# Kernel optimization log

Measured on AMD Instinct MI355X. Metric: run time of the kernel, lower is better.

The kernel has to match this reference:

```python
import jax, jax.numpy as jnp
import numpy as np

EMBED, HEADS, LEVELS, POINTS = 256, 8, 1, 4


def setup_inputs():
    key = jax.random.key(0)
    ks = jax.random.split(key, 8)
    B, NQ = 8, 8192
    Hh, Ww = 128, 128
    E, Hn, L, P = EMBED, HEADS, LEVELS, POINTS
    s = 1.0 / np.sqrt(E)
    return dict(
        query=jax.random.normal(ks[0], (B, NQ, E), jnp.float32),
        value=jax.random.normal(ks[1], (B, Hh * Ww, E), jnp.float32),
        ref_2d=jax.random.uniform(ks[2], (B, NQ, L, 2), dtype=jnp.float32),
        spatial_shapes=jnp.array([[Hh, Ww]], dtype=jnp.int32),
        W_off=jax.random.normal(ks[3], (E, Hn * L * P * 2), jnp.float32) * 0.01,
        b_off=jax.random.normal(ks[4], (Hn * L * P * 2,), jnp.float32) * 0.5,
        W_attn=jax.random.normal(ks[5], (E, Hn * L * P), jnp.float32) * s,
        b_attn=jnp.zeros((Hn * L * P,), jnp.float32),
        W_val=jax.random.normal(ks[6], (E, E), jnp.float32) * s,
        b_val=jnp.zeros((E,), jnp.float32),
        W_out=jax.random.normal(ks[7], (E, E), jnp.float32) * s,
        b_out=jnp.zeros((E,), jnp.float32),
    )


def _bilinear_sample(v, loc, Hl, Wl):
    # v: (B, Hn, Hl*Wl, dh); loc: (B, Hn, NQ, P, 2) normalized [0,1] (x, y)
    B, Hn, NQ, P, _ = loc.shape
    dh = v.shape[-1]
    # torch grid_sample(align_corners=False) pixel coords: p = loc * size - 0.5
    x = loc[..., 0] * Wl - 0.5
    y = loc[..., 1] * Hl - 0.5
    x0 = jnp.floor(x); y0 = jnp.floor(y)
    x1 = x0 + 1.0; y1 = y0 + 1.0
    wx1 = x - x0; wx0 = 1.0 - wx1
    wy1 = y - y0; wy0 = 1.0 - wy1

    def corner(xc, yc, w):
        valid = (xc >= 0) & (xc < Wl) & (yc >= 0) & (yc < Hl)  # zeros padding
        xi = jnp.clip(xc, 0, Wl - 1).astype(jnp.int32)
        yi = jnp.clip(yc, 0, Hl - 1).astype(jnp.int32)
        idx = (yi * Wl + xi).reshape(B, Hn, NQ * P, 1)
        vals = jnp.take_along_axis(v, idx, axis=2).reshape(B, Hn, NQ, P, dh)
        return vals * (w * valid.astype(v.dtype))[..., None]

    return (corner(x0, y0, wx0 * wy0) + corner(x1, y0, wx1 * wy0)
            + corner(x0, y1, wx0 * wy1) + corner(x1, y1, wx1 * wy1))


def _forward(query, value, ref_2d, W_off, b_off, W_attn, b_attn, W_val, b_val, W_out, b_out, shapes):
    B, NQ, E = query.shape
    Hn, L, P = HEADS, LEVELS, POINTS
    dh = E // Hn
    NV = value.shape[1]
    identity = query
    v = (value @ W_val + b_val).reshape(B, NV, Hn, dh)
    off = (query @ W_off + b_off).reshape(B, NQ, Hn, L, P, 2)
    attn = jax.nn.softmax((query @ W_attn + b_attn).reshape(B, NQ, Hn, L * P), axis=-1)
    attn = attn.reshape(B, NQ, Hn, L, P)
    # offset_normalizer = (W, H) per level
    norm = jnp.asarray(shapes[:, ::-1].copy(), dtype=query.dtype)
    loc = ref_2d[:, :, None, :, None, :] + off / norm[None, None, None, :, None, :]
    loc = jnp.transpose(loc, (0, 2, 1, 3, 4, 5))   # (B, Hn, NQ, L, P, 2)
    attn_t = jnp.transpose(attn, (0, 2, 1, 3, 4))  # (B, Hn, NQ, L, P)
    v_t = jnp.transpose(v, (0, 2, 1, 3))           # (B, Hn, NV, dh)
    starts = np.concatenate([[0], np.cumsum(shapes[:, 0] * shapes[:, 1])]).astype(np.int64)
    out = jnp.zeros((B, Hn, NQ, dh), query.dtype)
    for l in range(L):  # static small loop over feature levels
        Hl, Wl = int(shapes[l, 0]), int(shapes[l, 1])
        v_l = v_t[:, :, int(starts[l]):int(starts[l + 1]), :]
        samp = _bilinear_sample(v_l, loc[:, :, :, l], Hl, Wl)  # (B,Hn,NQ,P,dh)
        out = out + jnp.sum(samp * attn_t[:, :, :, l, :, None], axis=3)
    out = jnp.transpose(out, (0, 2, 1, 3)).reshape(B, NQ, E)
    # dropout is identity at eval time
    return out @ W_out + b_out + identity


def reference(query, value, ref_2d, spatial_shapes, W_off, b_off, W_attn, b_attn, W_val, b_val, W_out, b_out):
    shapes = np.asarray(jax.device_get(spatial_shapes))  # static level shapes
    return _forward(query, value, ref_2d, W_off, b_off, W_attn, b_attn, W_val, b_val, W_out, b_out, shapes)
```

## Files before the change

### kernel.cpp

```cpp
#include <hip/hip_runtime.h>

typedef short s16x8 __attribute__((ext_vector_type(8)));
typedef float f32x4 __attribute__((ext_vector_type(4)));

#define HN 8
#define PP 4
#define DH 32
#define NQc 8192
#define NVc 16384
#define EE 256
#define HWc 128

__device__ __forceinline__ unsigned short f2bf(float x) {
  unsigned u = __float_as_uint(x);
  u += 0x7FFF + ((u >> 16) & 1);
  return (unsigned short)(u >> 16);
}
__device__ __forceinline__ float bf2f(unsigned short h) {
  return __uint_as_float(((unsigned)h) << 16);
}

__global__ __launch_bounds__(256) void wprep(
    const float* __restrict__ Wval, const float* __restrict__ Wout,
    const float* __restrict__ Woff, const float* __restrict__ Wattn,
    const float* __restrict__ boff, const float* __restrict__ battn,
    unsigned short* __restrict__ wvt, unsigned short* __restrict__ wot,
    unsigned short* __restrict__ wct, float* __restrict__ bcat) {
  int g = blockIdx.x * 256 + threadIdx.x;
  if (g < 65536) {
    int n = g >> 8, k = g & 255;
    wvt[n * 256 + k] = f2bf(Wval[k * 256 + n]);
  } else if (g < 131072) {
    int g2 = g - 65536;
    int n = g2 >> 8, k = g2 & 255;
    wot[n * 256 + k] = f2bf(Wout[k * 256 + n]);
  } else if (g < 163840) {
    int g2 = g - 131072;
    int n = g2 >> 8, k = g2 & 255;
    float v = 0.f;
    if (n < 64) v = Woff[k * 64 + n];
    else if (n < 96) v = Wattn[k * 32 + (n - 64)];
    wct[n * 256 + k] = f2bf(v);
  } else if (g < 163968) {
    int c = g - 163840;
    bcat[c] = (c < 64) ? boff[c] : ((c < 96) ? battn[c - 64] : 0.f);
  }
}

#define MODE_VAL 0
#define MODE_PLAIN 1
#define MODE_OUT 2

template <int MODE>
struct SmemBytes { static constexpr int v = 36864; };
template <> struct SmemBytes<MODE_PLAIN> { static constexpr int v = 49664; };
template <> struct SmemBytes<MODE_OUT>   { static constexpr int v = 33792; };

template <int MODE, bool ABF16>
__global__ __launch_bounds__(256) void mfma_gemm(
    const void* __restrict__ Ain, const unsigned short* __restrict__ Wt,
    const float* __restrict__ bias, const float* __restrict__ resid,
    const float* __restrict__ ref2d, unsigned int* __restrict__ meta,
    void* __restrict__ outp) {
  __shared__ __align__(16) char smem[SmemBytes<MODE>::v];
  unsigned short* As = (unsigned short*)smem;
  unsigned short* Ws = As + 128 * 40;
  const int t = threadIdx.x;
  const int lane = t & 63, wave = t >> 6;
  const int lane15 = lane & 15, quad = lane >> 4;
  const int wr = wave >> 1, wc = wave & 1;
  const int bm = blockIdx.x * 128, bn = blockIdx.y * 128;

  f32x4 acc[4][4];
#pragma unroll
  for (int i = 0; i < 4; ++i)
#pragma unroll
    for (int j = 0; j < 4; ++j)
#pragma unroll
      for (int r = 0; r < 4; ++r) acc[i][j][r] = 0.f;

  const int ar = t >> 3, ac = (t & 7) * 4;
  const int wr2 = t >> 1, wcp = (t & 1) * 2;

  for (int k0 = 0; k0 < 256; k0 += 32) {
    float4 av[4];
    uint4 ab0, ab1;
    if (!ABF16) {
      const float* Af = (const float*)Ain;
#pragma unroll
      for (int i = 0; i < 4; ++i)
        av[i] = *(const float4*)(Af + (size_t)(bm + ar + i * 32) * 256 + k0 + ac);
    } else {
      const unsigned short* Ab = (const unsigned short*)Ain;
      ab0 = *(const uint4*)(Ab + (size_t)(bm + wr2) * 256 + k0 + wcp * 8);
      ab1 = *(const uint4*)(Ab + (size_t)(bm + wr2) * 256 + k0 + wcp * 8 + 8);
    }
    uint4 wv0 = *(const uint4*)(Wt + (size_t)(bn + wr2) * 256 + k0 + wcp * 8);
    uint4 wv1 = *(const uint4*)(Wt + (size_t)(bn + wr2) * 256 + k0 + wcp * 8 + 8);
    __syncthreads();
    if (!ABF16) {
#pragma unroll
      for (int i = 0; i < 4; ++i) {
        ushort4 c;
        c.x = f2bf(av[i].x); c.y = f2bf(av[i].y); c.z = f2bf(av[i].z); c.w = f2bf(av[i].w);
        *(ushort4*)&As[(ar + i * 32) * 40 + ac] = c;
      }
    } else {
      *(uint4*)&As[wr2 * 40 + wcp * 8] = ab0;
      *(uint4*)&As[wr2 * 40 + wcp * 8 + 8] = ab1;
    }
    *(uint4*)&Ws[wr2 * 40 + wcp * 8] = wv0;
    *(uint4*)&Ws[wr2 * 40 + wcp * 8 + 8] = wv1;
    __syncthreads();
    s16x8 af[4], bfr[4];
#pragma unroll
    for (int tm = 0; tm < 4; ++tm)
      af[tm] = *(const s16x8*)&As[(wr * 64 + tm * 16 + lane15) * 40 + quad * 8];
#pragma unroll
    for (int tn = 0; tn < 4; ++tn)
      bfr[tn] = *(const s16x8*)&Ws[(wc * 64 + tn * 16 + lane15) * 40 + quad * 8];
#pragma unroll
    for (int tm = 0; tm < 4; ++tm)
#pragma unroll
      for (int tn = 0; tn < 4; ++tn)
        acc[tm][tn] = __builtin_amdgcn_mfma_f32_16x16x32_bf16(af[tm], bfr[tn], acc[tm][tn], 0, 0, 0);
  }

  if (MODE == MODE_VAL) {
    unsigned short* Ct = (unsigned short*)smem;
    __syncthreads();
#pragma unroll
    for (int tm = 0; tm < 4; ++tm)
#pragma unroll
      for (int tn = 0; tn < 4; ++tn) {
        const int coll = wc * 64 + tn * 16 + lane15;
        const float bcol = bias[bn + coll];
#pragma unroll
        for (int r = 0; r < 4; ++r) {
          const int rowl = wr * 64 + tm * 16 + quad * 4 + r;
          Ct[rowl * 144 + coll] = f2bf(acc[tm][tn][r] + bcol);
        }
      }
    __syncthreads();
    unsigned short* outs = (unsigned short*)outp;
    const int b = bm >> 14, n0 = bm & (NVc - 1), hbase = bn >> 5;
#pragma unroll
    for (int i = 0; i < 8; ++i) {
      const int id = i * 256 + t;
      const int h4 = id >> 9, rem = id & 511, n = rem >> 2, c4 = rem & 3;
      uint4 v = *(const uint4*)&Ct[n * 144 + h4 * 32 + c4 * 8];
      *(uint4*)(outs + (((size_t)(b * HN + hbase + h4) * NVc + n0 + n) * DH + c4 * 8)) = v;
    }
  } else if (MODE == MODE_PLAIN) {
    float* Cf = (float*)smem;
    __syncthreads();
#pragma unroll
    for (int tm = 0; tm < 4; ++tm)
#pragma unroll
      for (int tn = 0; tn < 4; ++tn) {
        const int coll = wc * 64 + tn * 16 + lane15;
        if (coll < 96) {
          const float bcol = bias[coll];
#pragma unroll
          for (int r = 0; r < 4; ++r) {
            const int rowl = wr * 64 + tm * 16 + quad * 4 + r;
            Cf[rowl * 97 + coll] = acc[tm][tn][r] + bcol;
          }
        }
      }
    __syncthreads();
#pragma unroll
    for (int i = 0; i < 4; ++i) {
      const int task = i * 256 + t;
      const int h = task & 7, rowl = task >> 3;
      const int bq = bm + rowl;
      const float* row = Cf + rowl * 97;
      const float rx = ref2d[(size_t)bq * 2 + 0];
      const float ry = ref2d[(size_t)bq * 2 + 1];
      const float l0 = row[64 + h * 4 + 0], l1 = row[64 + h * 4 + 1];
      const float l2 = row[64 + h * 4 + 2], l3 = row[64 + h * 4 + 3];
      const float mx = fmaxf(fmaxf(l0, l1), fmaxf(l2, l3));
      float e0 = __expf(l0 - mx), e1 = __expf(l1 - mx), e2 = __expf(l2 - mx), e3 = __expf(l3 - mx);
      const float inv = 1.0f / (e0 + e1 + e2 + e3);
      float ee[4] = {e0, e1, e2, e3};
      unsigned int* m = meta + ((size_t)bq * 8 + h) * 20;
      uint4 pk;
      float4 wts[4];
#pragma unroll
      for (int p = 0; p < PP; ++p) {
        const float a = ee[p] * inv;
        const float ox = row[h * 8 + p * 2 + 0];
        const float oy = row[h * 8 + p * 2 + 1];
        const float x = (rx + ox * (1.0f / HWc)) * (float)HWc - 0.5f;
        const float y = (ry + oy * (1.0f / HWc)) * (float)HWc - 0.5f;
        const float x0f = floorf(x), y0f = floorf(y);
        const int x0 = (int)x0f, y0 = (int)y0f;
        const float wx1 = x - x0f, wx0 = 1.f - wx1;
        const float wy1 = y - y0f, wy0 = 1.f - wy1;
        const bool vx0 = (unsigned)x0 < (unsigned)HWc, vx1 = (unsigned)(x0 + 1) < (unsigned)HWc;
        const bool vy0 = (unsigned)y0 < (unsigned)HWc, vy1 = (unsigned)(y0 + 1) < (unsigned)HWc;
        const int xi0 = min(max(x0, 0), HWc - 1), xi1 = min(max(x0 + 1, 0), HWc - 1);
        const int yi0 = min(max(y0, 0), HWc - 1), yi1 = min(max(y0 + 1, 0), HWc - 1);
        const unsigned pv = (unsigned)xi0 | ((unsigned)yi0 << 8) | ((unsigned)xi1 << 16) | ((unsigned)yi1 << 24);
        if (p == 0) pk.x = pv; else if (p == 1) pk.y = pv; else if (p == 2) pk.z = pv; else pk.w = pv;
        float4 w;
        w.x = (vx0 && vy0) ? a * wx0 * wy0 : 0.f;
        w.y = (vx1 && vy0) ? a * wx1 * wy0 : 0.f;
        w.z = (vx0 && vy1) ? a * wx0 * wy1 : 0.f;
        w.w = (vx1 && vy1) ? a * wx1 * wy1 : 0.f;
        wts[p] = w;
      }
      *(uint4*)m = pk;
#pragma unroll
      for (int p = 0; p < PP; ++p) *(float4*)&m[4 + p * 4] = wts[p];
    }
  } else {
    float* Cf = (float*)smem;
    float* outf = (float*)outp;
#pragma unroll
    for (int pass = 0; pass < 2; ++pass) {
      __syncthreads();
      if (wr == pass) {
#pragma unroll
        for (int tm = 0; tm < 4; ++tm)
#pragma unroll
          for (int tn = 0; tn < 4; ++tn) {
            const int coll = wc * 64 + tn * 16 + lane15;
            const float bcol = bias[bn + coll];
#pragma unroll
            for (int r = 0; r < 4; ++r) {
              const int rowl = tm * 16 + quad * 4 + r;
              Cf[rowl * 132 + coll] = acc[tm][tn][r] + bcol;
            }
          }
      }
      __syncthreads();
#pragma unroll
      for (int i = 0; i < 8; ++i) {
        const int id = i * 256 + t;
        const int n = id >> 5, c = id & 31;
        const size_t row = (size_t)bm + pass * 64 + n;
        float4 v = *(const float4*)&Cf[n * 132 + c * 4];
        float4 rs = *(const float4*)(resid + row * 256 + bn + c * 4);
        v.x += rs.x; v.y += rs.y; v.z += rs.z; v.w += rs.w;
        *(float4*)(outf + row * 256 + bn + c * 4) = v;
      }
    }
  }
}

__global__ __launch_bounds__(256) void sample_kernel(
    const unsigned short* __restrict__ vbuf,
    const unsigned int* __restrict__ meta,
    unsigned short* __restrict__ outs) {
  const int t = threadIdx.x;
  const int d4 = (t & 7) << 2;
  const int ql = t >> 3;
  const int sl = blockIdx.x >> 8;
  const int qc = blockIdx.x & 255;
  const int b = sl >> 3;
  const int h = sl & 7;
  const int q = qc * 32 + ql;
  const size_t bq = (size_t)b * NQc + q;
  const unsigned int* m = meta + ((size_t)bq * 8 + h) * 20;
  const uint4 pk = *(const uint4*)m;
  const unsigned short* vb = vbuf + (size_t)sl * (NVc * DH) + d4;

  float4 acc = {0.f, 0.f, 0.f, 0.f};
#pragma unroll
  for (int p = 0; p < PP; ++p) {
    const unsigned P = (p == 0) ? pk.x : (p == 1) ? pk.y : (p == 2) ? pk.z : pk.w;
    const float4 w = *(const float4*)(m + 4 + p * 4);
    const int x0 = P & 255, y0 = (P >> 8) & 255, x1 = (P >> 16) & 255, y1 = P >> 24;
    const int r0 = y0 << 12, r1 = y1 << 12;
    const ushort4 v00 = *(const ushort4*)(vb + r0 + (x0 << 5));
    const ushort4 v10 = *(const ushort4*)(vb + r0 + (x1 << 5));
    const ushort4 v01 = *(const ushort4*)(vb + r1 + (x0 << 5));
    const ushort4 v11 = *(const ushort4*)(vb + r1 + (x1 << 5));
    acc.x += w.x * bf2f(v00.x); acc.y += w.x * bf2f(v00.y);
    acc.z += w.x * bf2f(v00.z); acc.w += w.x * bf2f(v00.w);
    acc.x += w.y * bf2f(v10.x); acc.y += w.y * bf2f(v10.y);
    acc.z += w.y * bf2f(v10.z); acc.w += w.y * bf2f(v10.w);
    acc.x += w.z * bf2f(v01.x); acc.y += w.z * bf2f(v01.y);
    acc.z += w.z * bf2f(v01.z); acc.w += w.z * bf2f(v01.w);
    acc.x += w.w * bf2f(v11.x); acc.y += w.w * bf2f(v11.y);
    acc.z += w.w * bf2f(v11.z); acc.w += w.w * bf2f(v11.w);
  }
  ushort4 o;
  o.x = f2bf(acc.x); o.y = f2bf(acc.y); o.z = f2bf(acc.z); o.w = f2bf(acc.w);
  *(ushort4*)(outs + bq * EE + h * DH + d4) = o;
}

extern "C" void kernel_launch(void* const* d_in, const int* in_sizes, int n_in,
                              void* d_out, int out_size, void* d_ws, size_t ws_size,
                              hipStream_t stream) {
  const float* query = (const float*)d_in[0];
  const float* value = (const float*)d_in[1];
  const float* ref2d = (const float*)d_in[2];
  const float* Woff  = (const float*)d_in[4];
  const float* boff  = (const float*)d_in[5];
  const float* Wattn = (const float*)d_in[6];
  const float* battn = (const float*)d_in[7];
  const float* Wval  = (const float*)d_in[8];
  const float* bval  = (const float*)d_in[9];
  const float* Wout  = (const float*)d_in[10];
  const float* bout  = (const float*)d_in[11];
  float* out = (float*)d_out;

  unsigned short* vbuf = (unsigned short*)d_ws;
  unsigned int* meta   = (unsigned int*)(vbuf + 33554432);
  unsigned short* sbuf = (unsigned short*)(meta + 10485760);
  unsigned short* wvt  = sbuf + 16777216;
  unsigned short* wot  = wvt + 65536;
  unsigned short* wct  = wot + 65536;
  float* bcat          = (float*)(wct + 32768);

  wprep<<<641, 256, 0, stream>>>(Wval, Wout, Woff, Wattn, boff, battn, wvt, wot, wct, bcat);

  mfma_gemm<MODE_VAL, false><<<dim3(1024, 2), 256, 0, stream>>>(
      (const void*)value, wvt, bval, nullptr, nullptr, nullptr, (void*)vbuf);

  mfma_gemm<MODE_PLAIN, false><<<dim3(512, 1), 256, 0, stream>>>(
      (const void*)query, wct, bcat, nullptr, ref2d, meta, nullptr);

  sample_kernel<<<16384, 256, 0, stream>>>(vbuf, meta, sbuf);

  mfma_gemm<MODE_OUT, true><<<dim3(512, 2), 256, 0, stream>>>(
      (const void*)sbuf, wot, bout, query, nullptr, nullptr, (void*)out);
}
```

Before: 417.2 us.

## Prefetch next K tile and write GEMM epilogues directly from transposed accumulators

The GEMM main loop now issues the global loads for the next K-slice right after the LDS barrier, so memory latency overlaps the MFMA work on the current slice. The MFMA operands are swapped so each lane holds four consecutive output columns of one row. This lets the value and output epilogues store vectorized results straight to global memory without staging through LDS and extra barriers. Shared memory shrinks for those modes, and the plain mode uses a padded float4-aligned stride. Holding the prefetched tile costs extra registers, and the direct stores may coalesce less well than the staged writes.

```diff
diff --git a/kernel.cpp b/kernel.cpp
--- a/kernel.cpp
+++ b/kernel.cpp
@@ -52,9 +52,8 @@
 #define MODE_OUT 2
 
 template <int MODE>
-struct SmemBytes { static constexpr int v = 36864; };
-template <> struct SmemBytes<MODE_PLAIN> { static constexpr int v = 49664; };
-template <> struct SmemBytes<MODE_OUT>   { static constexpr int v = 33792; };
+struct SmemBytes { static constexpr int v = 20480; };
+template <> struct SmemBytes<MODE_PLAIN> { static constexpr int v = 51200; };
 
 template <int MODE, bool ABF16>
 __global__ __launch_bounds__(256) void mfma_gemm(
@@ -82,21 +81,28 @@
   const int ar = t >> 3, ac = (t & 7) * 4;
   const int wr2 = t >> 1, wcp = (t & 1) * 2;
 
+  float4 av[4];
+  uint4 ab0, ab1, wv0, wv1;
+
+#define LOAD_TILE(K0)                                                          \
+  do {                                                                         \
+    if (!ABF16) {                                                              \
+      const float* Af = (const float*)Ain;                                     \
+      _Pragma("unroll") for (int i = 0; i < 4; ++i)                            \
+          av[i] = *(const float4*)(Af + (size_t)(bm + ar + i * 32) * 256 +     \
+                                   (K0) + ac);                                 \
+    } else {                                                                   \
+      const unsigned short* Ab = (const unsigned short*)Ain;                   \
+      ab0 = *(const uint4*)(Ab + (size_t)(bm + wr2) * 256 + (K0) + wcp * 8);   \
+      ab1 = *(const uint4*)(Ab + (size_t)(bm + wr2) * 256 + (K0) + wcp * 8 + 8); \
+    }                                                                          \
+    wv0 = *(const uint4*)(Wt + (size_t)(bn + wr2) * 256 + (K0) + wcp * 8);     \
+    wv1 = *(const uint4*)(Wt + (size_t)(bn + wr2) * 256 + (K0) + wcp * 8 + 8); \
+  } while (0)
+
+  LOAD_TILE(0);
+
   for (int k0 = 0; k0 < 256; k0 += 32) {
-    float4 av[4];
-    uint4 ab0, ab1;
-    if (!ABF16) {
-      const float* Af = (const float*)Ain;
-#pragma unroll
-      for (int i = 0; i < 4; ++i)
-        av[i] = *(const float4*)(Af + (size_t)(bm + ar + i * 32) * 256 + k0 + ac);
-    } else {
-      const unsigned short* Ab = (const unsigned short*)Ain;
-      ab0 = *(const uint4*)(Ab + (size_t)(bm + wr2) * 256 + k0 + wcp * 8);
-      ab1 = *(const uint4*)(Ab + (size_t)(bm + wr2) * 256 + k0 + wcp * 8 + 8);
-    }
-    uint4 wv0 = *(const uint4*)(Wt + (size_t)(bn + wr2) * 256 + k0 + wcp * 8);
-    uint4 wv1 = *(const uint4*)(Wt + (size_t)(bn + wr2) * 256 + k0 + wcp * 8 + 8);
     __syncthreads();
     if (!ABF16) {
 #pragma unroll
@@ -112,6 +118,7 @@
     *(uint4*)&Ws[wr2 * 40 + wcp * 8] = wv0;
     *(uint4*)&Ws[wr2 * 40 + wcp * 8 + 8] = wv1;
     __syncthreads();
+    if (k0 < 224) LOAD_TILE(k0 + 32);
     s16x8 af[4], bfr[4];
 #pragma unroll
     for (int tm = 0; tm < 4; ++tm)
@@ -123,58 +130,57 @@
     for (int tm = 0; tm < 4; ++tm)
 #pragma unroll
       for (int tn = 0; tn < 4; ++tn)
-        acc[tm][tn] = __builtin_amdgcn_mfma_f32_16x16x32_bf16(af[tm], bfr[tn], acc[tm][tn], 0, 0, 0);
+        acc[tm][tn] = __builtin_amdgcn_mfma_f32_16x16x32_bf16(bfr[tn], af[tm], acc[tm][tn], 0, 0, 0);
   }
+#undef LOAD_TILE
 
   if (MODE == MODE_VAL) {
-    unsigned short* Ct = (unsigned short*)smem;
-    __syncthreads();
-#pragma unroll
-    for (int tm = 0; tm < 4; ++tm)
-#pragma unroll
-      for (int tn = 0; tn < 4; ++tn) {
-        const int coll = wc * 64 + tn * 16 + lane15;
-        const float bcol = bias[bn + coll];
-#pragma unroll
-        for (int r = 0; r < 4; ++r) {
-          const int rowl = wr * 64 + tm * 16 + quad * 4 + r;
-          Ct[rowl * 144 + coll] = f2bf(acc[tm][tn][r] + bcol);
-        }
-      }
-    __syncthreads();
     unsigned short* outs = (unsigned short*)outp;
-    const int b = bm >> 14, n0 = bm & (NVc - 1), hbase = bn >> 5;
-#pragma unroll
-    for (int i = 0; i < 8; ++i) {
-      const int id = i * 256 + t;
-      const int h4 = id >> 9, rem = id & 511, n = rem >> 2, c4 = rem & 3;
-      uint4 v = *(const uint4*)&Ct[n * 144 + h4 * 32 + c4 * 8];
-      *(uint4*)(outs + (((size_t)(b * HN + hbase + h4) * NVc + n0 + n) * DH + c4 * 8)) = v;
+    const size_t b = (size_t)(bm >> 14);
+    const int n0 = bm & (NVc - 1);
+#pragma unroll
+    for (int tn = 0; tn < 4; ++tn) {
+      const int ch0 = bn + wc * 64 + tn * 16 + quad * 4;
+      const float4 b4 = *(const float4*)&bias[ch0];
+      const int h = ch0 >> 5, dh0 = ch0 & 31;
+#pragma unroll
+      for (int tm = 0; tm < 4; ++tm) {
+        const int n = n0 + wr * 64 + tm * 16 + lane15;
+        ushort4 o;
+        o.x = f2bf(acc[tm][tn][0] + b4.x);
+        o.y = f2bf(acc[tm][tn][1] + b4.y);
+        o.z = f2bf(acc[tm][tn][2] + b4.z);
+        o.w = f2bf(acc[tm][tn][3] + b4.w);
+        *(ushort4*)(outs + ((b * HN + h) * NVc + n) * DH + dh0) = o;
+      }
     }
   } else if (MODE == MODE_PLAIN) {
     float* Cf = (float*)smem;
     __syncthreads();
 #pragma unroll
-    for (int tm = 0; tm < 4; ++tm)
-#pragma unroll
-      for (int tn = 0; tn < 4; ++tn) {
-        const int coll = wc * 64 + tn * 16 + lane15;
-        if (coll < 96) {
-          const float bcol = bias[coll];
-#pragma unroll
-          for (int r = 0; r < 4; ++r) {
-            const int rowl = wr * 64 + tm * 16 + quad * 4 + r;
-            Cf[rowl * 97 + coll] = acc[tm][tn][r] + bcol;
-          }
+    for (int tn = 0; tn < 4; ++tn) {
+      const int col0 = wc * 64 + tn * 16 + quad * 4;
+      if (col0 < 96) {
+        const float4 b4 = *(const float4*)&bias[col0];
+#pragma unroll
+        for (int tm = 0; tm < 4; ++tm) {
+          const int m = wr * 64 + tm * 16 + lane15;
+          float4 v;
+          v.x = acc[tm][tn][0] + b4.x;
+          v.y = acc[tm][tn][1] + b4.y;
+          v.z = acc[tm][tn][2] + b4.z;
+          v.w = acc[tm][tn][3] + b4.w;
+          *(float4*)&Cf[m * 100 + col0] = v;
         }
       }
+    }
     __syncthreads();
 #pragma unroll
     for (int i = 0; i < 4; ++i) {
       const int task = i * 256 + t;
       const int h = task & 7, rowl = task >> 3;
       const int bq = bm + rowl;
-      const float* row = Cf + rowl * 97;
+      const float* row = Cf + rowl * 100;
       const float rx = ref2d[(size_t)bq * 2 + 0];
       const float ry = ref2d[(size_t)bq * 2 + 1];
       const float l0 = row[64 + h * 4 + 0], l1 = row[64 + h * 4 + 1];
@@ -215,35 +221,21 @@
       for (int p = 0; p < PP; ++p) *(float4*)&m[4 + p * 4] = wts[p];
     }
   } else {
-    float* Cf = (float*)smem;
     float* outf = (float*)outp;
 #pragma unroll
-    for (int pass = 0; pass < 2; ++pass) {
-      __syncthreads();
-      if (wr == pass) {
-#pragma unroll
-        for (int tm = 0; tm < 4; ++tm)
-#pragma unroll
-          for (int tn = 0; tn < 4; ++tn) {
-            const int coll = wc * 64 + tn * 16 + lane15;
-            const float bcol = bias[bn + coll];
-#pragma unroll
-            for (int r = 0; r < 4; ++r) {
-              const int rowl = tm * 16 + quad * 4 + r;
-              Cf[rowl * 132 + coll] = acc[tm][tn][r] + bcol;
-            }
-          }
-      }
-      __syncthreads();
-#pragma unroll
-      for (int i = 0; i < 8; ++i) {
-        const int id = i * 256 + t;
-        const int n = id >> 5, c = id & 31;
-        const size_t row = (size_t)bm + pass * 64 + n;
-        float4 v = *(const float4*)&Cf[n * 132 + c * 4];
-        float4 rs = *(const float4*)(resid + row * 256 + bn + c * 4);
-        v.x += rs.x; v.y += rs.y; v.z += rs.z; v.w += rs.w;
-        *(float4*)(outf + row * 256 + bn + c * 4) = v;
+    for (int tn = 0; tn < 4; ++tn) {
+      const int ch0 = bn + wc * 64 + tn * 16 + quad * 4;
+      const float4 b4 = *(const float4*)&bias[ch0];
+#pragma unroll
+      for (int tm = 0; tm < 4; ++tm) {
+        const size_t row = (size_t)bm + wr * 64 + tm * 16 + lane15;
+        float4 rs = *(const float4*)(resid + row * 256 + ch0);
+        float4 v;
+        v.x = acc[tm][tn][0] + b4.x + rs.x;
+        v.y = acc[tm][tn][1] + b4.y + rs.y;
+        v.z = acc[tm][tn][2] + b4.z + rs.z;
+        v.w = acc[tm][tn][3] + b4.w + rs.w;
+        *(float4*)(outf + row * 256 + ch0) = v;
       }
     }
   }
```

After: 424.0 us. About the same (+1.6%).
